# Kernel optimization log

Hardware: AMD Instinct MI355X
Metric: run time of the kernel (lower is better)

Reference implementation:

```python
import jax, jax.numpy as jnp
import numpy as np

NUM_NODES = 100000
NUM_EDGES = 1600000
NUM_GRAPHS = 512
F_IN = 128
HID = 128
N_CLASSES = 10
N_HIDDEN_LAYERS = 3


def _gcn_layer(x, W, b, src, dst, dinv, num_nodes):
    # PyG GCNConv: h = X W; out_i = sum_j norm_ij * h_j; out += bias
    h = x @ W                                  # [N, H]
    norm = dinv[src] * dinv[dst]               # [E'] edge norms (incl. self-loops)
    msg = h[src] * norm[:, None]               # [E', H] gather + scale
    out = jax.ops.segment_sum(msg, dst, num_segments=num_nodes)  # scatter-add
    return out + b


def setup_inputs() -> dict:
    key = jax.random.key(0)
    ks = jax.random.split(key, 12)
    x = jax.random.normal(ks[0], (NUM_NODES, F_IN), dtype=jnp.float32)
    edge_index = jax.random.randint(ks[1], (2, NUM_EDGES), 0, NUM_NODES, dtype=jnp.int64)
    batch = jnp.sort(jax.random.randint(ks[2], (NUM_NODES,), 0, NUM_GRAPHS, dtype=jnp.int64))
    s = 1.0 / np.sqrt(HID)
    W0 = jax.random.uniform(ks[3], (F_IN, HID), jnp.float32, -s, s)
    b0 = jnp.zeros((HID,), jnp.float32)
    W1 = jax.random.uniform(ks[4], (HID, HID), jnp.float32, -s, s)
    b1 = jnp.zeros((HID,), jnp.float32)
    W2 = jax.random.uniform(ks[5], (HID, HID), jnp.float32, -s, s)
    b2 = jnp.zeros((HID,), jnp.float32)
    W3 = jax.random.uniform(ks[6], (HID, HID), jnp.float32, -s, s)
    b3 = jnp.zeros((HID,), jnp.float32)
    Wl = jax.random.uniform(ks[7], (HID, N_CLASSES), jnp.float32, -s, s)
    bl = jnp.zeros((N_CLASSES,), jnp.float32)
    return {"x": x, "edge_index": edge_index, "batch": batch,
            "W0": W0, "b0": b0, "W1": W1, "b1": b1, "W2": W2, "b2": b2,
            "W3": W3, "b3": b3, "Wl": Wl, "bl": bl}


def reference(x, edge_index, batch, W0, b0, W1, b1, W2, b2, W3, b3, Wl, bl):
    n = x.shape[0]
    loops = jnp.arange(n, dtype=edge_index.dtype)
    src = jnp.concatenate([edge_index[0], loops])   # add self-loops
    dst = jnp.concatenate([edge_index[1], loops])
    deg = jax.ops.segment_sum(jnp.ones(dst.shape[0], x.dtype), dst, num_segments=n)
    dinv = jnp.where(deg > 0, jax.lax.rsqrt(deg), 0.0)

    h = jax.nn.relu(_gcn_layer(x, W0, b0, src, dst, dinv, n))
    for W, b in ((W1, b1), (W2, b2), (W3, b3)):
        h = jax.nn.relu(_gcn_layer(h, W, b, src, dst, dinv, n))

    # global_mean_pool over graph ids
    counts = jax.ops.segment_sum(jnp.ones(n, h.dtype), batch, num_segments=NUM_GRAPHS)
    pooled = jax.ops.segment_sum(h, batch, num_segments=NUM_GRAPHS)
    global_mean = pooled / jnp.maximum(counts, 1.0)[:, None]

    # dropout is identity in eval mode
    y = global_mean @ Wl + bl
    return (y, global_mean)
```

## Files before the change

kernel.cpp:

```cpp
#include <hip/hip_runtime.h>


#define ATOMIC_ADD_F32(p, v) __hip_atomic_fetch_add((p), (v), __ATOMIC_RELAXED, __HIP_MEMORY_SCOPE_AGENT)

constexpr int NG = 512;
constexpr float LO_SCALE = 4096.f;
constexpr float LO_INV   = 1.f / 4096.f;

typedef _Float16 half8 __attribute__((ext_vector_type(8)));
typedef float f32x4 __attribute__((ext_vector_type(4)));

__global__ __launch_bounds__(256) void k_deg_count_xcd(const int* __restrict__ dst,
                                                       int* __restrict__ deg,
                                                       int E, int N) {
    const int range = blockIdx.x & 7;
    const int chunk = blockIdx.x >> 3;
    const int nchunks = gridDim.x >> 3;
    const int csz = (E + nchunks - 1) / nchunks;
    const int lo = chunk * csz;
    const int hi = min(lo + csz, E);
    const int nr = N / 8;
    const int rlo = range * nr;
    const int rhi = (range == 7) ? N : rlo + nr;
    for (int i = lo + threadIdx.x; i < hi; i += 256) {
        int d = dst[i];
        if (d >= rlo && d < rhi) atomicAdd(&deg[d], 1);
    }
}

__global__ __launch_bounds__(256) void k_scan_local(const int* __restrict__ deg,
                                                    int* __restrict__ rowptr,
                                                    int* __restrict__ partials,
                                                    float* __restrict__ dinv, int N) {
    __shared__ int s[256];
    int t = threadIdx.x;
    int i = blockIdx.x * 256 + t;
    int dg = (i < N) ? deg[i] : 0;
    if (i < N) dinv[i] = rsqrtf((float)(dg + 1));
    s[t] = dg;
    __syncthreads();
#pragma unroll
    for (int off = 1; off < 256; off <<= 1) {
        int add = (t >= off) ? s[t - off] : 0;
        __syncthreads();
        s[t] += add;
        __syncthreads();
    }
    if (i < N) rowptr[i] = s[t] - dg;
    if (t == 255) partials[blockIdx.x] = s[t];
}

__global__ __launch_bounds__(512) void k_scan_partials(int* __restrict__ partials, int nblk) {
    __shared__ int s[512];
    int t = threadIdx.x;
    int v = (t < nblk) ? partials[t] : 0;
    s[t] = v;
    __syncthreads();
#pragma unroll
    for (int off = 1; off < 512; off <<= 1) {
        int add = (t >= off) ? s[t - off] : 0;
        __syncthreads();
        s[t] += add;
        __syncthreads();
    }
    if (t < nblk) partials[t] = s[t] - v;
}

__global__ __launch_bounds__(256) void k_scan_apply(const int* __restrict__ deg,
                                                    int* __restrict__ rowptr,
                                                    int* __restrict__ cursor,
                                                    const int* __restrict__ partials, int N) {
    int i = blockIdx.x * 256 + threadIdx.x;
    if (i < N) {
        int r = rowptr[i] + partials[blockIdx.x];
        rowptr[i] = r;
        cursor[i] = r;
        if (i == N - 1) rowptr[N] = r + deg[i];
    }
}

__global__ __launch_bounds__(256) void k_csr_fill_xcd(const int* __restrict__ src,
                                                      const int* __restrict__ dst,
                                                      int* __restrict__ cursor,
                                                      int* __restrict__ csr_src,
                                                      int E, int N) {
    const int range = blockIdx.x & 7;
    const int chunk = blockIdx.x >> 3;
    const int nchunks = gridDim.x >> 3;
    const int csz = (E + nchunks - 1) / nchunks;
    const int lo = chunk * csz;
    const int hi = min(lo + csz, E);
    const int nr = N / 8;
    const int rlo = range * nr;
    const int rhi = (range == 7) ? N : rlo + nr;
    for (int i = lo + threadIdx.x; i < hi; i += 256) {
        int d = dst[i];
        if (d >= rlo && d < rhi) {
            int pos = atomicAdd(&cursor[d], 1);
            csr_src[pos] = src[i];
        }
    }
}

struct WSplitArgs {
    const float* W[4];
    _Float16* Wth[4];
    _Float16* Wtl[4];
};
__global__ __launch_bounds__(256) void k_wsplit4(WSplitArgs a) {
    int idx = blockIdx.x * 256 + threadIdx.x;
    int layer = idx >> 14;
    int e = idx & 16383;
    int k = e >> 7, c = e & 127;
    float w = a.W[layer][e];
    _Float16 hi = (_Float16)w;
    float lo = (w - (float)hi) * LO_SCALE;
    int ctile = c >> 4, lr = c & 15;
    int ks = k >> 5, q = (k >> 3) & 3, ee = k & 7;
    int pos = (((ctile * 4 + ks) * 64) + q * 16 + lr) * 8 + ee;
    a.Wth[layer][pos] = hi;
    a.Wtl[layer][pos] = (_Float16)lo;
}

template <int AFP32>
__global__ __launch_bounds__(256) void k_gemm_f16(const void* __restrict__ Aptr,
                                                  const _Float16* __restrict__ Wth,
                                                  const _Float16* __restrict__ Wtl,
                                                  const float* __restrict__ dinv,
                                                  _Float16* __restrict__ Hh, int N) {
    __shared__ _Float16 Hs[64][136];
    const int tid = threadIdx.x;
    const int wave = tid >> 6;
    const int l = tid & 63;
    const int wrow = wave & 1;
    const int wcol = wave >> 1;
    const int lr = l & 15;
    const int q = l >> 4;

    const int blk_row0 = blockIdx.x * 64;
    const int row_base = blk_row0 + wrow * 32;
    const int c_base = wcol * 64;

    f32x4 acch[2][4], accl[2][4];
#pragma unroll
    for (int rt = 0; rt < 2; ++rt)
#pragma unroll
        for (int ct = 0; ct < 4; ++ct) {
            acch[rt][ct] = (f32x4){0.f, 0.f, 0.f, 0.f};
            accl[rt][ct] = (f32x4){0.f, 0.f, 0.f, 0.f};
        }

#pragma unroll
    for (int ks = 0; ks < 4; ++ks) {
        const int koff = ks * 32 + q * 8;

        half8 bh[4], bl[4];
#pragma unroll
        for (int ct = 0; ct < 4; ++ct) {
            size_t off = (size_t)(((wcol * 4 + ct) * 4 + ks) * 64 + l) * 8;
            bh[ct] = *(const half8*)(Wth + off);
            bl[ct] = *(const half8*)(Wtl + off);
        }

        half8 a[2];
#pragma unroll
        for (int rt = 0; rt < 2; ++rt) {
            int r = row_base + rt * 16 + lr;
            if (r >= N) r = N - 1;
            if constexpr (AFP32) {
                const float* xp = (const float*)Aptr + (size_t)r * 128 + koff;
                float4 f0 = *(const float4*)xp;
                float4 f1 = *(const float4*)(xp + 4);
                half8 h;
                h[0] = (_Float16)f0.x; h[1] = (_Float16)f0.y;
                h[2] = (_Float16)f0.z; h[3] = (_Float16)f0.w;
                h[4] = (_Float16)f1.x; h[5] = (_Float16)f1.y;
                h[6] = (_Float16)f1.z; h[7] = (_Float16)f1.w;
                a[rt] = h;
            } else {
                a[rt] = *(const half8*)((const _Float16*)Aptr + (size_t)r * 128 + koff);
            }
        }

#pragma unroll
        for (int rt = 0; rt < 2; ++rt)
#pragma unroll
            for (int ct = 0; ct < 4; ++ct) {
                acch[rt][ct] = __builtin_amdgcn_mfma_f32_16x16x32_f16(a[rt], bh[ct], acch[rt][ct], 0, 0, 0);
                accl[rt][ct] = __builtin_amdgcn_mfma_f32_16x16x32_f16(a[rt], bl[ct], accl[rt][ct], 0, 0, 0);
            }
    }

#pragma unroll
    for (int rt = 0; rt < 2; ++rt) {
        int lrow0 = wrow * 32 + rt * 16 + q * 4;
        int gr0 = blk_row0 + lrow0;
        float dv[4];
#pragma unroll
        for (int j = 0; j < 4; ++j) dv[j] = (gr0 + j < N) ? dinv[gr0 + j] : 0.f;
#pragma unroll
        for (int ct = 0; ct < 4; ++ct) {
            int col = c_base + ct * 16 + lr;
#pragma unroll
            for (int j = 0; j < 4; ++j) {
                float v = fmaf(accl[rt][ct][j], LO_INV, acch[rt][ct][j]);
                Hs[lrow0 + j][col] = (_Float16)(v * dv[j]);
            }
        }
    }
    __syncthreads();

#pragma unroll
    for (int it = 0; it < 8; ++it) {
        int idx = it * 256 + tid;
        int row = idx >> 5, c2 = idx & 31;
        int gr = blk_row0 + row;
        if (gr < N) {
            uint2 v = *(const uint2*)&Hs[row][c2 * 4];
            ((uint2*)Hh)[(size_t)gr * 32 + c2] = v;
        }
    }
}

__global__ __launch_bounds__(256) void k_aggregate_f16(const int* __restrict__ csr_src,
                                                       const int* __restrict__ rowptr,
                                                       const float* __restrict__ dinv,
                                                       const _Float16* __restrict__ Hh,
                                                       const float* __restrict__ bias,
                                                       _Float16* __restrict__ Ah, int N) {
    int d = blockIdx.x * 4 + (threadIdx.x >> 6);
    if (d >= N) return;
    const int lane = threadIdx.x & 63;
    const unsigned* Hu = (const unsigned*)Hh;

    int beg = rowptr[d], end = rowptr[d + 1];
    union PK { unsigned u; _Float16 h[2]; };

    PK sv; sv.u = Hu[(size_t)d * 64 + lane];
    float ax = (float)sv.h[0];
    float ay = (float)sv.h[1];

    int j = beg;
    for (; j + 7 < end; j += 8) {
        int s[8]; PK v[8];
#pragma unroll
        for (int u = 0; u < 8; ++u) s[u] = csr_src[j + u];
#pragma unroll
        for (int u = 0; u < 8; ++u) v[u].u = Hu[(size_t)s[u] * 64 + lane];
#pragma unroll
        for (int u = 0; u < 8; ++u) {
            ax += (float)v[u].h[0];
            ay += (float)v[u].h[1];
        }
    }
    for (; j < end; ++j) {
        PK v; v.u = Hu[(size_t)csr_src[j] * 64 + lane];
        ax += (float)v.h[0];
        ay += (float)v.h[1];
    }

    float dd = dinv[d];
    float2 b2 = ((const float2*)bias)[lane];
    ax = fmaxf(fmaf(dd, ax, b2.x), 0.f);
    ay = fmaxf(fmaf(dd, ay, b2.y), 0.f);

    PK o; o.h[0] = (_Float16)ax; o.h[1] = (_Float16)ay;
    ((unsigned*)Ah)[(size_t)d * 64 + lane] = o.u;
}

__global__ __launch_bounds__(128) void k_pool(const _Float16* __restrict__ A,
                                              const int* __restrict__ batch,
                                              float* __restrict__ pooled,
                                              float* __restrict__ counts, int N) {
    int k = threadIdx.x;
    int i0 = blockIdx.x * 64;
    if (i0 >= N) return;
    int iend = min(i0 + 64, N);
    float acc = 0.f;
    int cnt = 0;
    int cur = batch[i0];
    for (int i = i0; i < iend; ++i) {
        int g = batch[i];
        if (g != cur) {
            ATOMIC_ADD_F32(&pooled[cur * 128 + k], acc);
            if (k == 0) ATOMIC_ADD_F32(&counts[cur], (float)cnt);
            acc = 0.f; cnt = 0; cur = g;
        }
        acc += (float)A[(size_t)i * 128 + k];
        cnt++;
    }
    ATOMIC_ADD_F32(&pooled[cur * 128 + k], acc);
    if (k == 0) ATOMIC_ADD_F32(&counts[cur], (float)cnt);
}

__global__ __launch_bounds__(128) void k_finalize(const float* __restrict__ pooled,
                                                  const float* __restrict__ counts,
                                                  const float* __restrict__ Wl,
                                                  const float* __restrict__ bl,
                                                  float* __restrict__ out) {
    int g = blockIdx.x;
    int t = threadIdx.x;
    __shared__ float m[128];
    float c = fmaxf(counts[g], 1.f);
    float mean = pooled[g * 128 + t] / c;
    out[NG * 10 + g * 128 + t] = mean;
    m[t] = mean;
    __syncthreads();
    if (t < 10) {
        float acc = bl[t];
#pragma unroll 16
        for (int k = 0; k < 128; ++k) acc = fmaf(m[k], Wl[k * 10 + t], acc);
        out[g * 10 + t] = acc;
    }
}

extern "C" void kernel_launch(void* const* d_in, const int* in_sizes, int n_in,
                              void* d_out, int out_size, void* d_ws, size_t ws_size,
                              hipStream_t stream) {
    const float* x     = (const float*)d_in[0];
    const int*   ei    = (const int*)d_in[1];
    const int*   batch = (const int*)d_in[2];
    const float* Wt[4] = { (const float*)d_in[3], (const float*)d_in[5],
                           (const float*)d_in[7], (const float*)d_in[9] };
    const float* bt[4] = { (const float*)d_in[4], (const float*)d_in[6],
                           (const float*)d_in[8], (const float*)d_in[10] };
    const float* Wl = (const float*)d_in[11];
    const float* bl = (const float*)d_in[12];
    float* out = (float*)d_out;

    const int N = in_sizes[0] / 128;
    const int E = in_sizes[1] / 2;
    const int* src = ei;
    const int* dst = ei + E;

    char* p = (char*)d_ws;
    _Float16* Hh    = (_Float16*)p;  p += (size_t)N * 128 * 2;
    _Float16* Ah    = (_Float16*)p;  p += (size_t)N * 128 * 2;
    float* dinv     = (float*)p;     p += (size_t)N * 4;
    int*   deg      = (int*)p;       p += (size_t)N * 4;
    int*   rowptr   = (int*)p;       p += (size_t)(N + 1) * 4;
    int*   cursor   = (int*)p;       p += (size_t)N * 4;
    int*   csr_src  = (int*)p;       p += (size_t)E * 4;
    int*   partials = (int*)p;       p += 512 * 4;
    float* pooled   = (float*)p;     p += (size_t)NG * 128 * 4;
    float* counts   = (float*)p;     p += (size_t)NG * 4;
    _Float16* Wsp   = (_Float16*)p;  p += 4 * 2 * 128 * 128 * 2;

    const int nblk = (N + 255) / 256;

    hipMemsetAsync(deg, 0, (size_t)N * 4, stream);
    k_deg_count_xcd<<<2048, 256, 0, stream>>>(dst, deg, E, N);

    k_scan_local<<<nblk, 256, 0, stream>>>(deg, rowptr, partials, dinv, N);
    k_scan_partials<<<1, 512, 0, stream>>>(partials, nblk);
    k_scan_apply<<<nblk, 256, 0, stream>>>(deg, rowptr, cursor, partials, N);
    k_csr_fill_xcd<<<2048, 256, 0, stream>>>(src, dst, cursor, csr_src, E, N);

    WSplitArgs wa;
    _Float16* Wth[4]; _Float16* Wtl[4];
    for (int l = 0; l < 4; ++l) {
        Wth[l] = Wsp + (size_t)l * 2 * 16384;
        Wtl[l] = Wth[l] + 16384;
        wa.W[l] = Wt[l];
        wa.Wth[l] = Wth[l];
        wa.Wtl[l] = Wtl[l];
    }
    k_wsplit4<<<256, 256, 0, stream>>>(wa);

    const int gemm_blocks = (N + 63) / 64;
    const int agg_blocks = (N + 3) / 4;
    k_gemm_f16<1><<<gemm_blocks, 256, 0, stream>>>(x, Wth[0], Wtl[0], dinv, Hh, N);
    k_aggregate_f16<<<agg_blocks, 256, 0, stream>>>(csr_src, rowptr, dinv, Hh, bt[0], Ah, N);
    for (int l = 1; l < 4; ++l) {
        k_gemm_f16<0><<<gemm_blocks, 256, 0, stream>>>(Ah, Wth[l], Wtl[l], dinv, Hh, N);
        k_aggregate_f16<<<agg_blocks, 256, 0, stream>>>(csr_src, rowptr, dinv, Hh, bt[l], Ah, N);
    }

    hipMemsetAsync(pooled, 0, (size_t)(NG * 128 + NG) * 4, stream);
    k_pool<<<(N + 63) / 64, 128, 0, stream>>>(Ah, batch, pooled, counts, N);
    k_finalize<<<NG, 128, 0, stream>>>(pooled, counts, Wl, bl, out);
}
```

Measured before the change: 570.7 us.

## Pre-partition edges into destination-range buckets before degree count and CSR fill

Adds a partition pass that scatters (src,dst) pairs into 8 buckets by destination range, using shared-memory counters and global cursors. The degree and CSR-fill kernels then read only their own bucket instead of each of the 8 range groups scanning the full edge list, which cuts redundant reads of dst/src. The cost is an extra partition pass with atomics and an extra 8-byte-per-edge buffer. Bucket capacity is fixed at 1.5x the average bucket size, so a skewed input could overflow it.

Measured after the change: 645.0 us. +13.0%, slower.

```diff
diff --git a/kernel.cpp b/kernel.cpp
--- a/kernel.cpp
+++ b/kernel.cpp
@@ -10,22 +10,47 @@
 typedef _Float16 half8 __attribute__((ext_vector_type(8)));
 typedef float f32x4 __attribute__((ext_vector_type(4)));
 
-__global__ __launch_bounds__(256) void k_deg_count_xcd(const int* __restrict__ dst,
-                                                       int* __restrict__ deg,
-                                                       int E, int N) {
-    const int range = blockIdx.x & 7;
+__global__ __launch_bounds__(256) void k_partition(const int* __restrict__ src,
+                                                   const int* __restrict__ dst,
+                                                   int* __restrict__ gcur,
+                                                   int2* __restrict__ buck,
+                                                   int E, int N, int bcap) {
+    __shared__ int cnt[8];
+    __shared__ int base[8];
+    const int nr = N / 8;
+    const int tiles = (E + 255) / 256;
+    for (int tile = blockIdx.x; tile < tiles; tile += gridDim.x) {
+        int i = tile * 256 + threadIdx.x;
+        if (threadIdx.x < 8) cnt[threadIdx.x] = 0;
+        __syncthreads();
+        int r = 0, pos = 0, s = 0, d = 0;
+        bool valid = (i < E);
+        if (valid) {
+            d = dst[i]; s = src[i];
+            r = d / nr; if (r > 7) r = 7;
+            pos = atomicAdd(&cnt[r], 1);
+        }
+        __syncthreads();
+        if (threadIdx.x < 8) base[threadIdx.x] = atomicAdd(&gcur[threadIdx.x], cnt[threadIdx.x]);
+        __syncthreads();
+        if (valid) buck[(size_t)r * bcap + base[r] + pos] = make_int2(s, d);
+        __syncthreads();
+    }
+}
+
+__global__ __launch_bounds__(256) void k_deg_bucket(const int2* __restrict__ buck,
+                                                    const int* __restrict__ gcur,
+                                                    int* __restrict__ deg, int bcap) {
+    const int r = blockIdx.x & 7;
     const int chunk = blockIdx.x >> 3;
-    const int nchunks = gridDim.x >> 3;
-    const int csz = (E + nchunks - 1) / nchunks;
+    const int nch = gridDim.x >> 3;
+    const int cnt = gcur[r];
+    const int csz = (cnt + nch - 1) / nch;
     const int lo = chunk * csz;
-    const int hi = min(lo + csz, E);
-    const int nr = N / 8;
-    const int rlo = range * nr;
-    const int rhi = (range == 7) ? N : rlo + nr;
-    for (int i = lo + threadIdx.x; i < hi; i += 256) {
-        int d = dst[i];
-        if (d >= rlo && d < rhi) atomicAdd(&deg[d], 1);
-    }
+    const int hi = min(lo + csz, cnt);
+    const int2* b = buck + (size_t)r * bcap;
+    for (int i = lo + threadIdx.x; i < hi; i += 256)
+        atomicAdd(&deg[b[i].y], 1);
 }
 
 __global__ __launch_bounds__(256) void k_scan_local(const int* __restrict__ deg,
@@ -79,26 +104,22 @@
     }
 }
 
-__global__ __launch_bounds__(256) void k_csr_fill_xcd(const int* __restrict__ src,
-                                                      const int* __restrict__ dst,
-                                                      int* __restrict__ cursor,
-                                                      int* __restrict__ csr_src,
-                                                      int E, int N) {
-    const int range = blockIdx.x & 7;
+__global__ __launch_bounds__(256) void k_fill_bucket(const int2* __restrict__ buck,
+                                                     const int* __restrict__ gcur,
+                                                     int* __restrict__ cursor,
+                                                     int* __restrict__ csr_src, int bcap) {
+    const int r = blockIdx.x & 7;
     const int chunk = blockIdx.x >> 3;
-    const int nchunks = gridDim.x >> 3;
-    const int csz = (E + nchunks - 1) / nchunks;
+    const int nch = gridDim.x >> 3;
+    const int cnt = gcur[r];
+    const int csz = (cnt + nch - 1) / nch;
     const int lo = chunk * csz;
-    const int hi = min(lo + csz, E);
-    const int nr = N / 8;
-    const int rlo = range * nr;
-    const int rhi = (range == 7) ? N : rlo + nr;
+    const int hi = min(lo + csz, cnt);
+    const int2* b = buck + (size_t)r * bcap;
     for (int i = lo + threadIdx.x; i < hi; i += 256) {
-        int d = dst[i];
-        if (d >= rlo && d < rhi) {
-            int pos = atomicAdd(&cursor[d], 1);
-            csr_src[pos] = src[i];
-        }
+        int2 e = b[i];
+        int pos = atomicAdd(&cursor[e.y], 1);
+        csr_src[pos] = e.x;
     }
 }
 
@@ -332,6 +353,7 @@
     const int E = in_sizes[1] / 2;
     const int* src = ei;
     const int* dst = ei + E;
+    const int bcap = E / 8 + E / 16;
 
     char* p = (char*)d_ws;
     _Float16* Hh    = (_Float16*)p;  p += (size_t)N * 128 * 2;
@@ -345,16 +367,22 @@
     float* pooled   = (float*)p;     p += (size_t)NG * 128 * 4;
     float* counts   = (float*)p;     p += (size_t)NG * 4;
     _Float16* Wsp   = (_Float16*)p;  p += 4 * 2 * 128 * 128 * 2;
+    int*   gcur     = (int*)p;       p += 8 * 4;
+    int2*  buck     = (int2*)p;      p += (size_t)8 * bcap * 8;
 
     const int nblk = (N + 255) / 256;
 
+    hipMemsetAsync(gcur, 0, 8 * 4, stream);
     hipMemsetAsync(deg, 0, (size_t)N * 4, stream);
-    k_deg_count_xcd<<<2048, 256, 0, stream>>>(dst, deg, E, N);
+    k_partition<<<2048, 256, 0, stream>>>(src, dst, gcur, buck, E, N, bcap);
+
+    k_deg_bucket<<<2048, 256, 0, stream>>>(buck, gcur, deg, bcap);
 
     k_scan_local<<<nblk, 256, 0, stream>>>(deg, rowptr, partials, dinv, N);
     k_scan_partials<<<1, 512, 0, stream>>>(partials, nblk);
     k_scan_apply<<<nblk, 256, 0, stream>>>(deg, rowptr, cursor, partials, N);
-    k_csr_fill_xcd<<<2048, 256, 0, stream>>>(src, dst, cursor, csr_src, E, N);
+
+    k_fill_bucket<<<2048, 256, 0, stream>>>(buck, gcur, cursor, csr_src, bcap);
 
     WSplitArgs wa;
     _Float16* Wth[4]; _Float16* Wtl[4];
```
